# Kernel optimization log

Hardware: AMD Instinct MI355X
Metric: run time of the kernel (lower is better)

Reference implementation:

```python
import jax, jax.numpy as jnp
import numpy as np

N = 50000   # nodes
E = 600000  # edges (avg degree 12)
D = 128     # node feature dim (input == hidden so residual applies)
R = 7       # num_relation
G = 32      # num graphs in the batch
L = 3       # layers
W_SCALE = 0.02


def setup_inputs() -> dict:
    key = jax.random.key(0)
    ks = jax.random.split(key, 5 + 2 * L)
    inp = {
        "x": jax.random.normal(ks[0], (N, D), jnp.float32),
        "node_in": jax.random.randint(ks[1], (E,), 0, N),
        "node_out": jax.random.randint(ks[2], (E,), 0, N),
        "relation": jax.random.randint(ks[3], (E,), 0, R),
        "edge_weight": jnp.ones((E,), jnp.float32),
        "node2graph": jnp.sort(jax.random.randint(ks[4], (N,), 0, G)),
        "num_node": N,
        "num_graphs": G,
    }
    for i in range(L):
        inp[f"sl_w{i}"] = jax.random.normal(ks[5 + 2 * i], (D, D), jnp.float32) * W_SCALE
        inp[f"sl_b{i}"] = jnp.zeros((D,), jnp.float32)
        inp[f"lin_w{i}"] = jax.random.normal(ks[6 + 2 * i], (R * D, D), jnp.float32) * W_SCALE
        inp[f"lin_b{i}"] = jnp.zeros((D,), jnp.float32)
    return inp


def _gearnet(x, edge_weight, params, node_in, node_out, relation, node2graph,
             num_node, num_graphs):
    # relation-keyed scatter index: node_out * R + relation
    idx = node_out * R + relation  # [E]
    h = x
    for (sl_w, sl_b, lin_w, lin_b) in params:
        din = h.shape[1]
        msg = h[node_in] * edge_weight[:, None]                           # [E, din] gather
        agg = jax.ops.segment_sum(msg, idx, num_segments=num_node * R)    # [N*R, din] scatter_add
        upd = agg.reshape(num_node, R * din)                              # [N, R*din]
        out = jax.nn.relu(upd @ lin_w + lin_b + h @ sl_w + sl_b)          # combine: linear + self_loop, relu
        h = out + h                                                        # short_cut residual (shapes match)
    node_feature = h
    graph_feature = jax.ops.segment_sum(node_feature, node2graph, num_segments=num_graphs)  # SumReadout
    return graph_feature, node_feature


def reference(x, node_in, node_out, relation, edge_weight, node2graph,
              sl_w0, sl_b0, lin_w0, lin_b0,
              sl_w1, sl_b1, lin_w1, lin_b1,
              sl_w2, sl_b2, lin_w2, lin_b2,
              num_node, num_graphs):
    params = [(sl_w0, sl_b0, lin_w0, lin_b0),
              (sl_w1, sl_b1, lin_w1, lin_b1),
              (sl_w2, sl_b2, lin_w2, lin_b2)]
    return _gearnet(x, edge_weight, params, node_in, node_out, relation,
                    node2graph, num_node, num_graphs)
```

## Files before the change

kernel.cpp:

```cpp
#include <hip/hip_runtime.h>
#include <hip/hip_bf16.h>

#define NN 50000
#define EE 600000
#define DD 128
#define RR 7
#define SS 8
#define GG 32
#define NSEG (NN * RR)
#define NB1 ((NSEG + 1023) / 1024)

typedef float f32x4 __attribute__((ext_vector_type(4)));
typedef float f32x2 __attribute__((ext_vector_type(2)));
typedef short short8 __attribute__((ext_vector_type(8)));
typedef unsigned short u16x8 __attribute__((ext_vector_type(8)));

static __device__ __forceinline__ unsigned short f2bf(float f) {
    union { float f; unsigned u; } v; v.f = f;
    unsigned r = v.u + 0x7fff + ((v.u >> 16) & 1);
    return (unsigned short)(r >> 16);
}
static __device__ __forceinline__ float bf2f(unsigned short u) {
    union { unsigned u; float f; } v; v.u = ((unsigned)u) << 16;
    return v.f;
}

__global__ void prep_w2(const float* __restrict__ lin_w, const float* __restrict__ sl_w,
                        const float* __restrict__ lin_b, const float* __restrict__ sl_b,
                        unsigned short* __restrict__ Wt2, float* __restrict__ bias) {
    int idx = blockIdx.x * 256 + threadIdx.x;
    if (idx < DD) bias[idx] = lin_b[idx] + sl_b[idx];
    if (idx >= 1024 * DD) return;
    int j = idx >> 7;
    int k = idx & 127;
    int slot = j >> 7, dout = j & 127;
    float w = (slot < 7) ? lin_w[(slot * DD + k) * DD + dout] : sl_w[k * DD + dout];
    Wt2[(size_t)j * DD + k] = f2bf(w);
}

__global__ void zero_ints(int* __restrict__ p, int n) {
    int i = blockIdx.x * 256 + threadIdx.x;
    if (i < n) p[i] = 0;
}

__global__ void hist(const int* __restrict__ node_out, const int* __restrict__ rel,
                     int* __restrict__ counts) {
    int e = blockIdx.x * 256 + threadIdx.x;
    if (e >= EE) return;
    atomicAdd(&counts[node_out[e] * RR + rel[e]], 1);
}

__global__ __launch_bounds__(256) void scan1(const int* __restrict__ counts,
                                             int* __restrict__ start, int* __restrict__ bsum) {
    __shared__ int s[256];
    int tid = threadIdx.x;
    int base = blockIdx.x * 1024 + tid * 4;
    int v[4], sum = 0;
    #pragma unroll
    for (int j = 0; j < 4; ++j) {
        v[j] = (base + j < NSEG) ? counts[base + j] : 0;
        sum += v[j];
    }
    s[tid] = sum; __syncthreads();
    for (int off = 1; off < 256; off <<= 1) {
        int t = (tid >= off) ? s[tid - off] : 0;
        __syncthreads();
        s[tid] += t;
        __syncthreads();
    }
    int run = s[tid] - sum;
    if (tid == 255) bsum[blockIdx.x] = s[255];
    #pragma unroll
    for (int j = 0; j < 4; ++j) {
        if (base + j < NSEG) { start[base + j] = run; run += v[j]; }
    }
}

__global__ __launch_bounds__(512) void scan2(int* __restrict__ bsum) {
    __shared__ int s[512];
    int tid = threadIdx.x;
    int v = (tid < NB1) ? bsum[tid] : 0;
    s[tid] = v; __syncthreads();
    for (int off = 1; off < 512; off <<= 1) {
        int t = (tid >= off) ? s[tid - off] : 0;
        __syncthreads();
        s[tid] += t;
        __syncthreads();
    }
    if (tid < NB1) bsum[tid] = s[tid] - v;
}

__global__ void scan3(const int* __restrict__ start, const int* __restrict__ bsum,
                      const int* __restrict__ counts, int2* __restrict__ segd) {
    int i = blockIdx.x * 256 + threadIdx.x;
    if (i < NSEG) segd[i] = make_int2(start[i] + bsum[i >> 10], counts[i]);
}

__global__ void fill(const int* __restrict__ node_in, const int* __restrict__ node_out,
                     const int* __restrict__ rel, const float* __restrict__ ew,
                     const int2* __restrict__ segd, int* __restrict__ cursor,
                     int2* __restrict__ edges) {
    int e = blockIdx.x * 256 + threadIdx.x;
    if (e >= EE) return;
    int seg = node_out[e] * RR + rel[e];
    int pos = segd[seg].x + atomicAdd(&cursor[seg], 1);
    edges[pos] = make_int2((rel[e] << 16) | node_in[e], __float_as_int(ew[e]));
}

__global__ void init_hb(const float* __restrict__ x, unsigned short* __restrict__ hb) {
    int t = blockIdx.x * 256 + threadIdx.x;
    if (t >= NN * 32) return;
    f32x4 v = ((const f32x4*)x)[t];
    unsigned long long pack = (unsigned long long)f2bf(v.x)
                            | ((unsigned long long)f2bf(v.y) << 16)
                            | ((unsigned long long)f2bf(v.z) << 32)
                            | ((unsigned long long)f2bf(v.w) << 48);
    ((unsigned long long*)hb)[t] = pack;
}

__global__ __launch_bounds__(256) void gemm_p(
        const unsigned short* __restrict__ hb,
        const unsigned short* __restrict__ Wt2,
        unsigned short* __restrict__ P) {
    __shared__ unsigned short sA[128 * 128];
    int tid = threadIdx.x;
    int bm0 = (blockIdx.x >> 3) * 128;
    int bj0 = (blockIdx.x & 7) * 128;
    #pragma unroll
    for (int it = 0; it < 8; ++it) {
        int cid = it * 256 + tid;
        int row = cid >> 4, c = cid & 15;
        int gr = bm0 + row;
        u16x8 t8 = {};
        if (gr < NN) t8 = *(const u16x8*)(hb + (size_t)gr * DD + c * 8);
        ((u16x8*)sA)[row * 16 + (c ^ (row & 7))] = t8;
    }
    __syncthreads();
    int wid = tid >> 6, lane = tid & 63;
    int wr = wid >> 1, wc = wid & 1;
    int lm = lane & 15, lg = lane >> 4;
    f32x4 acc[4][4] = {};
    #pragma unroll
    for (int ks = 0; ks < 4; ++ks) {
        short8 af[4], bfr[4];
        #pragma unroll
        for (int mi = 0; mi < 4; ++mi) {
            int row = wr * 64 + mi * 16 + lm;
            af[mi] = ((const short8*)sA)[row * 16 + ((ks * 4 + lg) ^ (row & 7))];
        }
        #pragma unroll
        for (int ni = 0; ni < 4; ++ni)
            bfr[ni] = *(const short8*)(Wt2 + (size_t)(bj0 + wc * 64 + ni * 16 + lm) * DD + ks * 32 + lg * 8);
        #pragma unroll
        for (int mi = 0; mi < 4; ++mi)
            #pragma unroll
            for (int ni = 0; ni < 4; ++ni)
                acc[mi][ni] = __builtin_amdgcn_mfma_f32_16x16x32_bf16(af[mi], bfr[ni], acc[mi][ni], 0, 0, 0);
    }
    #pragma unroll
    for (int mi = 0; mi < 4; ++mi) {
        #pragma unroll
        for (int v = 0; v < 4; ++v) {
            int gm = bm0 + wr * 64 + mi * 16 + lg * 4 + v;
            if (gm >= NN) continue;
            #pragma unroll
            for (int ni = 0; ni < 4; ++ni) {
                int j = bj0 + wc * 64 + ni * 16 + lm;
                P[(size_t)gm * 1024 + j] = f2bf(acc[mi][ni][v]);
            }
        }
    }
}

__global__ __launch_bounds__(256) void gather_p(
        const unsigned short* __restrict__ P,
        const int2* __restrict__ segd,
        const int2* __restrict__ edges,
        const float* __restrict__ bias,
        const float* __restrict__ hprev,
        float* __restrict__ hout,
        unsigned short* __restrict__ hb_next,
        int write_next) {
    int tid = threadIdx.x;
    int wv = tid >> 6, lane = tid & 63;
    int node = blockIdx.x * 4 + wv;
    int st = segd[node * RR].x;
    int2 s6 = segd[node * RR + 6];
    int end = s6.x + s6.y;

    float ax = 0.f, ay = 0.f;
    int2 r0 = edges[st];
    int2 r1 = edges[st + 1];
    int2 r2 = edges[st + 2];
    unsigned hv0 = *(const unsigned*)(P + (size_t)(((r0.x & 0xFFFF) << 3) | (r0.x >> 16)) * DD + lane * 2);
    unsigned hv1 = *(const unsigned*)(P + (size_t)(((r1.x & 0xFFFF) << 3) | (r1.x >> 16)) * DD + lane * 2);
    for (int i = st; i < end; ++i) {
        int2 r3 = edges[i + 3];
        unsigned hv2 = *(const unsigned*)(P + (size_t)(((r2.x & 0xFFFF) << 3) | (r2.x >> 16)) * DD + lane * 2);
        float w = __int_as_float(r0.y);
        ax += bf2f((unsigned short)(hv0 & 0xFFFF)) * w;
        ay += bf2f((unsigned short)(hv0 >> 16)) * w;
        r0 = r1; r1 = r2; r2 = r3;
        hv0 = hv1; hv1 = hv2;
    }
    unsigned hs = *(const unsigned*)(P + ((size_t)node * 8 + 7) * DD + lane * 2);
    float bx = bias[lane * 2], by = bias[lane * 2 + 1];
    f32x2 hp = ((const f32x2*)hprev)[(size_t)node * 64 + lane];
    float vx = fmaxf(ax + bf2f((unsigned short)(hs & 0xFFFF)) + bx, 0.f) + hp.x;
    float vy = fmaxf(ay + bf2f((unsigned short)(hs >> 16)) + by, 0.f) + hp.y;
    ((f32x2*)hout)[(size_t)node * 64 + lane] = (f32x2){vx, vy};
    if (write_next)
        ((unsigned*)hb_next)[(size_t)node * 64 + lane] =
            (unsigned)f2bf(vx) | ((unsigned)f2bf(vy) << 16);
}

__global__ void zero_gf(float* gf) {
    int t = blockIdx.x * 256 + threadIdx.x;
    if (t < GG * DD) gf[t] = 0.f;
}

__global__ __launch_bounds__(256) void readout(const float* __restrict__ h,
                                               const int* __restrict__ n2g,
                                               float* __restrict__ gf) {
    int c0 = blockIdx.x * 128;
    int rg = threadIdx.x >> 5, d4 = threadIdx.x & 31;
    f32x4 acc = {0.f, 0.f, 0.f, 0.f};
    int cur = -1;
    #pragma unroll 4
    for (int it = 0; it < 16; ++it) {
        int row = c0 + it * 8 + rg;
        if (row >= NN) break;
        int g = n2g[row];
        if (g != cur) {
            if (cur >= 0) {
                atomicAdd(&gf[cur * DD + d4 * 4 + 0], acc.x);
                atomicAdd(&gf[cur * DD + d4 * 4 + 1], acc.y);
                atomicAdd(&gf[cur * DD + d4 * 4 + 2], acc.z);
                atomicAdd(&gf[cur * DD + d4 * 4 + 3], acc.w);
            }
            cur = g;
            acc = (f32x4){0.f, 0.f, 0.f, 0.f};
        }
        acc += ((const f32x4*)h)[(size_t)row * 32 + d4];
    }
    if (cur >= 0) {
        atomicAdd(&gf[cur * DD + d4 * 4 + 0], acc.x);
        atomicAdd(&gf[cur * DD + d4 * 4 + 1], acc.y);
        atomicAdd(&gf[cur * DD + d4 * 4 + 2], acc.z);
        atomicAdd(&gf[cur * DD + d4 * 4 + 3], acc.w);
    }
}

extern "C" void kernel_launch(void* const* d_in, const int* in_sizes, int n_in,
                              void* d_out, int out_size, void* d_ws, size_t ws_size,
                              hipStream_t stream) {
    const float* x      = (const float*)d_in[0];
    const int* node_in  = (const int*)d_in[1];
    const int* node_out = (const int*)d_in[2];
    const int* relation = (const int*)d_in[3];
    const float* ew     = (const float*)d_in[4];
    const int* n2g      = (const int*)d_in[5];
    const float* sl_w[3]  = {(const float*)d_in[8],  (const float*)d_in[12], (const float*)d_in[16]};
    const float* sl_b[3]  = {(const float*)d_in[9],  (const float*)d_in[13], (const float*)d_in[17]};
    const float* lin_w[3] = {(const float*)d_in[10], (const float*)d_in[14], (const float*)d_in[18]};
    const float* lin_b[3] = {(const float*)d_in[11], (const float*)d_in[15], (const float*)d_in[19]};

    float* out = (float*)d_out;
    float* gf = out;
    float* nf = out + GG * DD;

    char* ws = (char*)d_ws;
    size_t off = 0;
    unsigned short* P  = (unsigned short*)(ws + off); off += (size_t)NN * 1024 * 2;
    unsigned short* hb0 = (unsigned short*)(ws + off); off += (size_t)NN * DD * 2;
    unsigned short* hb1 = (unsigned short*)(ws + off); off += (size_t)NN * DD * 2;
    float* hA   = (float*)(ws + off);            off += (size_t)NN * DD * 4;
    unsigned short* Wt2 = (unsigned short*)(ws + off); off += (size_t)3 * 1024 * DD * 2;
    float* bias = (float*)(ws + off);            off += 3 * DD * 4;
    int* counts = (int*)(ws + off);              off += (size_t)NSEG * 4;
    int* cursor = (int*)(ws + off);              off += (size_t)NSEG * 4;
    int* start  = (int*)(ws + off);              off += (size_t)NSEG * 4;
    int2* segd  = (int2*)(ws + off);             off += (size_t)NSEG * 8;
    int* bsum   = (int*)(ws + off);              off += 512 * 4;
    int2* edges = (int2*)(ws + off);             off += (size_t)(EE + 8) * 8;

    for (int l = 0; l < 3; ++l)
        prep_w2<<<512, 256, 0, stream>>>(lin_w[l], sl_w[l], lin_b[l], sl_b[l],
                                         Wt2 + (size_t)l * 1024 * DD, bias + l * DD);

    zero_ints<<<(2 * NSEG + 255) / 256, 256, 0, stream>>>(counts, 2 * NSEG);
    zero_ints<<<1, 64, 0, stream>>>((int*)(edges + EE), 16);
    hist<<<(EE + 255) / 256, 256, 0, stream>>>(node_out, relation, counts);
    scan1<<<NB1, 256, 0, stream>>>(counts, start, bsum);
    scan2<<<1, 512, 0, stream>>>(bsum);
    scan3<<<(NSEG + 255) / 256, 256, 0, stream>>>(start, bsum, counts, segd);
    fill<<<(EE + 255) / 256, 256, 0, stream>>>(node_in, node_out, relation, ew,
                                               segd, cursor, edges);
    init_hb<<<(NN * 32) / 256, 256, 0, stream>>>(x, hb0);

    const float* hcur = x;
    float* houts[3] = { nf, hA, nf };
    unsigned short* hbs[2] = { hb0, hb1 };
    for (int l = 0; l < 3; ++l) {
        gemm_p<<<((NN + 127) / 128) * 8, 256, 0, stream>>>(
            hbs[l & 1], Wt2 + (size_t)l * 1024 * DD, P);
        gather_p<<<NN / 4, 256, 0, stream>>>(
            P, segd, edges, bias + l * DD, hcur, houts[l],
            hbs[(l + 1) & 1], l < 2 ? 1 : 0);
        hcur = houts[l];
    }
    zero_gf<<<(GG * DD + 255) / 256, 256, 0, stream>>>(gf);
    readout<<<(NN + 127) / 128, 256, 0, stream>>>(nf, n2g, gf);
}
```

Before: 433.3 us.

## Keep A fragments in registers and loop over all column blocks per workgroup

The GEMM producing the per-relation projections P now assigns one workgroup per 128-row tile. It loads that tile's A fragments straight from global memory into registers once and loops over all 8 column blocks of the weight matrix. This drops the shared-memory staging, the barrier and the repeated reloading of A across 8 separate workgroups. The trade-off is 8x fewer workgroups (about 391 on a 256-CU part), more registers per thread, and serialized column blocks within each workgroup, which may reduce occupancy and parallelism.

```diff
diff --git a/kernel.cpp b/kernel.cpp
--- a/kernel.cpp
+++ b/kernel.cpp
@@ -122,51 +122,49 @@
         const unsigned short* __restrict__ hb,
         const unsigned short* __restrict__ Wt2,
         unsigned short* __restrict__ P) {
-    __shared__ unsigned short sA[128 * 128];
     int tid = threadIdx.x;
-    int bm0 = (blockIdx.x >> 3) * 128;
-    int bj0 = (blockIdx.x & 7) * 128;
-    #pragma unroll
-    for (int it = 0; it < 8; ++it) {
-        int cid = it * 256 + tid;
-        int row = cid >> 4, c = cid & 15;
-        int gr = bm0 + row;
-        u16x8 t8 = {};
-        if (gr < NN) t8 = *(const u16x8*)(hb + (size_t)gr * DD + c * 8);
-        ((u16x8*)sA)[row * 16 + (c ^ (row & 7))] = t8;
-    }
-    __syncthreads();
     int wid = tid >> 6, lane = tid & 63;
     int wr = wid >> 1, wc = wid & 1;
     int lm = lane & 15, lg = lane >> 4;
-    f32x4 acc[4][4] = {};
+    int bm0 = blockIdx.x * 128;
+
+    short8 af[4][4];
     #pragma unroll
-    for (int ks = 0; ks < 4; ++ks) {
-        short8 af[4], bfr[4];
+    for (int mi = 0; mi < 4; ++mi) {
+        int gr = bm0 + wr * 64 + mi * 16 + lm;
+        #pragma unroll
+        for (int ks = 0; ks < 4; ++ks) {
+            short8 t = {};
+            if (gr < NN) t = *(const short8*)(hb + (size_t)gr * DD + ks * 32 + lg * 8);
+            af[mi][ks] = t;
+        }
+    }
+    for (int cb = 0; cb < 8; ++cb) {
+        f32x4 acc[4][4] = {};
+        #pragma unroll
+        for (int ks = 0; ks < 4; ++ks) {
+            short8 bfr[4];
+            #pragma unroll
+            for (int ni = 0; ni < 4; ++ni)
+                bfr[ni] = *(const short8*)(Wt2 + (size_t)(cb * 128 + wc * 64 + ni * 16 + lm) * DD
+                                           + ks * 32 + lg * 8);
+            #pragma unroll
+            for (int mi = 0; mi < 4; ++mi)
+                #pragma unroll
+                for (int ni = 0; ni < 4; ++ni)
+                    acc[mi][ni] = __builtin_amdgcn_mfma_f32_16x16x32_bf16(af[mi][ks], bfr[ni], acc[mi][ni], 0, 0, 0);
+        }
         #pragma unroll
         for (int mi = 0; mi < 4; ++mi) {
-            int row = wr * 64 + mi * 16 + lm;
-            af[mi] = ((const short8*)sA)[row * 16 + ((ks * 4 + lg) ^ (row & 7))];
-        }
-        #pragma unroll
-        for (int ni = 0; ni < 4; ++ni)
-            bfr[ni] = *(const short8*)(Wt2 + (size_t)(bj0 + wc * 64 + ni * 16 + lm) * DD + ks * 32 + lg * 8);
-        #pragma unroll
-        for (int mi = 0; mi < 4; ++mi)
             #pragma unroll
-            for (int ni = 0; ni < 4; ++ni)
-                acc[mi][ni] = __builtin_amdgcn_mfma_f32_16x16x32_bf16(af[mi], bfr[ni], acc[mi][ni], 0, 0, 0);
-    }
-    #pragma unroll
-    for (int mi = 0; mi < 4; ++mi) {
-        #pragma unroll
-        for (int v = 0; v < 4; ++v) {
-            int gm = bm0 + wr * 64 + mi * 16 + lg * 4 + v;
-            if (gm >= NN) continue;
-            #pragma unroll
-            for (int ni = 0; ni < 4; ++ni) {
-                int j = bj0 + wc * 64 + ni * 16 + lm;
-                P[(size_t)gm * 1024 + j] = f2bf(acc[mi][ni][v]);
+            for (int v = 0; v < 4; ++v) {
+                int gm = bm0 + wr * 64 + mi * 16 + lg * 4 + v;
+                if (gm >= NN) continue;
+                #pragma unroll
+                for (int ni = 0; ni < 4; ++ni) {
+                    int j = cb * 128 + wc * 64 + ni * 16 + lm;
+                    P[(size_t)gm * 1024 + j] = f2bf(acc[mi][ni][v]);
+                }
             }
         }
     }
@@ -302,7 +300,7 @@
     float* houts[3] = { nf, hA, nf };
     unsigned short* hbs[2] = { hb0, hb1 };
     for (int l = 0; l < 3; ++l) {
-        gemm_p<<<((NN + 127) / 128) * 8, 256, 0, stream>>>(
+        gemm_p<<<(NN + 127) / 128, 256, 0, stream>>>(
             hbs[l & 1], Wt2 + (size_t)l * 1024 * DD, P);
         gather_p<<<NN / 4, 256, 0, stream>>>(
             P, segd, edges, bias + l * DD, hcur, houts[l],
```

Measured after the change: 402.0 us. 1.08x faster.
